# Performance work log

Measured on AMD Instinct MI355X. Metric: run time of the kernel, lower is better.

## Reference

```python
import jax, jax.numpy as jnp
import numpy as np

EMBED_DIM = 1024
NUM_HEADS = 16
HEAD_DIM = EMBED_DIM // NUM_HEADS
SCALE = HEAD_DIM ** -0.5


def setup_inputs() -> dict:
    key = jax.random.key(0)
    ks = jax.random.split(key, 9)
    B, S, D = 4, 2048, EMBED_DIM
    w_std = 1.0 / np.sqrt(D)
    x = jax.random.normal(ks[0], (B, S, D), dtype=jnp.float32)
    Wq = jax.random.uniform(ks[1], (D, D), jnp.float32, -w_std, w_std)
    bq = jax.random.uniform(ks[2], (D,), jnp.float32, -w_std, w_std)
    Wk = jax.random.uniform(ks[3], (D, D), jnp.float32, -w_std, w_std)
    bk = jax.random.uniform(ks[4], (D,), jnp.float32, -w_std, w_std)
    Wv = jax.random.uniform(ks[5], (D, D), jnp.float32, -w_std, w_std)
    bv = jax.random.uniform(ks[6], (D,), jnp.float32, -w_std, w_std)
    Wo = jax.random.uniform(ks[7], (D, D), jnp.float32, -w_std, w_std)
    bo = jax.random.uniform(ks[8], (D,), jnp.float32, -w_std, w_std)
    return {"x": x, "Wq": Wq, "bq": bq, "Wk": Wk, "bk": bk,
            "Wv": Wv, "bv": bv, "Wo": Wo, "bo": bo}


def reference(x, Wq, bq, Wk, bk, Wv, bv, Wo, bo):
    B, S, D = x.shape
    H, Dh = NUM_HEADS, HEAD_DIM
    # projections; Linear stores weight as [out,in] -> y = x @ W.T + b,
    # here W is stored as [D, D] used as x @ W + b (equivalent param'zation)
    q = (x @ Wq + bq).reshape(B, S, H, Dh).transpose(0, 2, 1, 3)  # [B,H,S,Dh]
    k = (x @ Wk + bk).reshape(B, S, H, Dh).transpose(0, 2, 1, 3)
    v = (x @ Wv + bv).reshape(B, S, H, Dh).transpose(0, 2, 1, 3)
    scores = jnp.einsum("bhqd,bhkd->bhqk", q, k) * SCALE  # [B,H,S,S]
    attn = jax.nn.softmax(scores, axis=-1)  # dropout is identity in eval mode
    out = jnp.einsum("bhqk,bhkd->bhqd", attn, v)  # [B,H,S,Dh]
    out = out.transpose(0, 2, 1, 3).reshape(B, S, D)
    return out @ Wo + bo
```

## Files before the change

### kernel.cpp

```cpp
#include <hip/hip_runtime.h>
#include <stdint.h>
#include <stddef.h>


typedef __attribute__((ext_vector_type(8)))  short          s16x8;
typedef __attribute__((ext_vector_type(8)))  unsigned short u16x8;
typedef __attribute__((ext_vector_type(4)))  unsigned short u16x4;
typedef __attribute__((ext_vector_type(4)))  float          f32x4;
typedef __attribute__((ext_vector_type(16))) float          f32x16;

#define DMODEL 1024
#define SEQ    2048
#define NHEAD  16
#define DHEAD  64
#define NTOK   8192
#define QSCALE 0.1803368801111244f

#define MFMA_B16(a, b, c) __builtin_amdgcn_mfma_f32_16x16x32_bf16((a), (b), (c), 0, 0, 0)
#define MFMA32(a, b, c)   __builtin_amdgcn_mfma_f32_32x32x16_bf16((a), (b), (c), 0, 0, 0)

__device__ __forceinline__ float bf2f(unsigned short u) {
  union { unsigned int i; float f; } v; v.i = ((unsigned int)u) << 16; return v.f;
}
__device__ __forceinline__ unsigned short f2bf(float f) {
  union { float f; unsigned int i; } v; v.f = f;
  unsigned int r = v.i + 0x7FFFu + ((v.i >> 16) & 1u);
  return (unsigned short)(r >> 16);
}
__device__ __forceinline__ float fexp2(float x) {
#if __has_builtin(__builtin_amdgcn_exp2f)
  return __builtin_amdgcn_exp2f(x);
#else
  return exp2f(x);
#endif
}
__device__ __forceinline__ unsigned int cvtpk(float a, float b) {
  unsigned int r;
  asm("v_cvt_pk_bf16_f32 %0, %1, %2" : "=v"(r) : "v"(a), "v"(b));
  return r;
}

__device__ __forceinline__ void gld16(const unsigned short* g, unsigned short* l) {
  __builtin_amdgcn_global_load_lds(
      (const __attribute__((address_space(1))) void*)g,
      (__attribute__((address_space(3))) void*)l, 16, 0, 0);
}

__global__ void detect_fp32(const unsigned short* __restrict__ w, int* __restrict__ flag) {
  __shared__ int cnt;
  if (threadIdx.x == 0) cnt = 0;
  __syncthreads();
  int local = 0;
  for (int i = threadIdx.x; i < 8192; i += 256) {
    const unsigned short v = w[i];
    if ((v & 0x7F80u) >= 0x3F80u) local++;
  }
  atomicAdd(&cnt, local);
  __syncthreads();
  if (threadIdx.x == 0) *flag = (cnt >= 128) ? 1 : 0;
}

__global__ void norm_vec4(const void* __restrict__ s0, const void* __restrict__ s1,
                          const void* __restrict__ s2, const void* __restrict__ s3,
                          unsigned short* __restrict__ d0, unsigned short* __restrict__ d1,
                          unsigned short* __restrict__ d2, unsigned short* __restrict__ d3,
                          const int* __restrict__ flag) {
  const int fl = *flag;
  const int v = blockIdx.y;
  const void* src = (v == 0) ? s0 : (v == 1) ? s1 : (v == 2) ? s2 : s3;
  unsigned short* dst = (v == 0) ? d0 : (v == 1) ? d1 : (v == 2) ? d2 : d3;
  const int i = blockIdx.x * 256 + threadIdx.x;
  dst[i] = fl ? f2bf(((const float*)src)[i]) : ((const unsigned short*)src)[i];
}

__global__ __launch_bounds__(256) void norm_x(const void* __restrict__ src,
                                              unsigned short* __restrict__ dst,
                                              const int* __restrict__ flag) {
  const int fl = *flag;
  const size_t i = ((size_t)blockIdx.x * 256 + threadIdx.x) * 8;
  if (fl) {
    const float* s = (const float*)src + i;
    u16x8 o;
#pragma unroll
    for (int j = 0; j < 8; ++j) o[j] = f2bf(s[j]);
    *(u16x8*)(dst + i) = o;
  } else {
    *(u16x8*)(dst + i) = *(const u16x8*)((const unsigned short*)src + i);
  }
}

__global__ __launch_bounds__(256) void transpose4(const void* __restrict__ i0,
                                                  const void* __restrict__ i1,
                                                  const void* __restrict__ i2,
                                                  const void* __restrict__ i3,
                                                  unsigned short* __restrict__ o0,
                                                  unsigned short* __restrict__ o1,
                                                  unsigned short* __restrict__ o2,
                                                  unsigned short* __restrict__ o3,
                                                  const int* __restrict__ flag) {
  __shared__ unsigned short tile[64][65];
  const int z = blockIdx.z;
  const void* in = (z == 0) ? i0 : (z == 1) ? i1 : (z == 2) ? i2 : i3;
  unsigned short* out = (z == 0) ? o0 : (z == 1) ? o1 : (z == 2) ? o2 : o3;
  const int fl = *flag;
  const int tx = threadIdx.x;
  const int ty = threadIdx.y;
  const int bx = blockIdx.x * 64;
  const int by = blockIdx.y * 64;
  const float* inf = (const float*)in;
  const unsigned short* inu = (const unsigned short*)in;
#pragma unroll
  for (int i = 0; i < 16; ++i) {
    const int r = i * 4 + ty;
    const size_t idx = (size_t)(by + r) * DMODEL + bx + tx;
    tile[r][tx] = fl ? f2bf(inf[idx]) : inu[idx];
  }
  __syncthreads();
#pragma unroll
  for (int i = 0; i < 16; ++i) {
    const int r = i * 4 + ty;
    out[(size_t)(bx + r) * DMODEL + by + tx] = tile[tx][r];
  }
}

template <int MODE>
__global__ __launch_bounds__(256) void gemm_bt(const unsigned short* __restrict__ A,
                                               const unsigned short* __restrict__ Bt,
                                               const unsigned short* __restrict__ bias0,
                                               const unsigned short* __restrict__ bias1,
                                               unsigned short* __restrict__ C0,
                                               unsigned short* __restrict__ C1,
                                               float* __restrict__ Cf) {
  __shared__ __align__(16) unsigned short As[128 * 32];
  __shared__ __align__(16) unsigned short Bs[128 * 32];

  const int t = threadIdx.x;
  const int wv = t >> 6;
  const int lane = t & 63;
  const int q4 = lane >> 4;
  const int c  = lane & 15;
  const int wm = wv >> 1;
  const int wn = wv & 1;
  const int m0 = blockIdx.x * 128;
  const int n0 = blockIdx.y * 128;

  f32x4 acc[4][4];
#pragma unroll
  for (int i = 0; i < 4; ++i)
#pragma unroll
    for (int j = 0; j < 4; ++j) acc[i][j] = (f32x4){0.f, 0.f, 0.f, 0.f};

  const int ch0 = wv * 128 + lane;
  const int ch1 = ch0 + 64;
  const unsigned short* Ag0 = A  + (size_t)(m0 + (ch0 >> 2)) * DMODEL + (ch0 & 3) * 8;
  const unsigned short* Ag1 = A  + (size_t)(m0 + (ch1 >> 2)) * DMODEL + (ch1 & 3) * 8;
  const unsigned short* Bg0 = Bt + (size_t)(n0 + (ch0 >> 2)) * DMODEL + (ch0 & 3) * 8;
  const unsigned short* Bg1 = Bt + (size_t)(n0 + (ch1 >> 2)) * DMODEL + (ch1 & 3) * 8;
  unsigned short* Al0 = As + (wv * 2 + 0) * 512;
  unsigned short* Al1 = As + (wv * 2 + 1) * 512;
  unsigned short* Bl0 = Bs + (wv * 2 + 0) * 512;
  unsigned short* Bl1 = Bs + (wv * 2 + 1) * 512;

  for (int k0 = 0; k0 < DMODEL; k0 += 32) {
    gld16(Ag0 + k0, Al0);
    gld16(Ag1 + k0, Al1);
    gld16(Bg0 + k0, Bl0);
    gld16(Bg1 + k0, Bl1);
    __syncthreads();

    s16x8 af[4], bfr[4];
#pragma unroll
    for (int i = 0; i < 4; ++i)
      af[i] = *(const s16x8*)(As + (wm * 64 + i * 16 + c) * 32 + q4 * 8);
#pragma unroll
    for (int j = 0; j < 4; ++j)
      bfr[j] = *(const s16x8*)(Bs + (wn * 64 + j * 16 + c) * 32 + q4 * 8);
    __builtin_amdgcn_s_setprio(1);
#pragma unroll
    for (int i = 0; i < 4; ++i)
#pragma unroll
      for (int j = 0; j < 4; ++j) acc[i][j] = MFMA_B16(af[i], bfr[j], acc[i][j]);
    __builtin_amdgcn_s_setprio(0);
    __syncthreads();
  }

  if (MODE == 2) {
#pragma unroll
    for (int i = 0; i < 4; ++i) {
#pragma unroll
      for (int rg = 0; rg < 4; ++rg) {
        const int m = m0 + wm * 64 + i * 16 + q4 * 4 + rg;
        const float bval = bf2f(bias0[m]);
#pragma unroll
        for (int j = 0; j < 4; ++j) {
          const int n = n0 + wn * 64 + j * 16 + c;
          C0[(((size_t)(n >> 11) * 1024 + m) << 11) + (n & 2047)] =
              f2bf(acc[i][j][rg] + bval);
        }
      }
    }
  } else {
#pragma unroll
    for (int j = 0; j < 4; ++j) {
      const int n = n0 + wn * 64 + j * 16 + c;
      float bval;
      if (MODE == 0) {
        bval = bf2f(bias0[n]);
      } else {
        bval = bf2f((n < 1024) ? bias0[n] : bias1[n & 1023]);
      }
#pragma unroll
      for (int i = 0; i < 4; ++i) {
#pragma unroll
        for (int rg = 0; rg < 4; ++rg) {
          const int m = m0 + wm * 64 + i * 16 + q4 * 4 + rg;
          const float oval = acc[i][j][rg] + bval;
          if (MODE == 0) {
            Cf[(size_t)m * DMODEL + n] = oval;
          } else {
            const int d = n & 1023;
            const int h = d >> 6, dh = d & 63;
            const int b = m >> 11, s = m & 2047;
            const size_t idx = ((((size_t)b * NHEAD + h) * SEQ + s) << 6) + dh;
            if (n < 1024) C0[idx] = f2bf(oval * QSCALE);
            else          C1[idx] = f2bf(oval);
          }
        }
      }
    }
  }
}

__global__ void copyout(const float* __restrict__ X, void* __restrict__ out,
                        const int* __restrict__ flag) {
  const int fl = *flag;
  const size_t i = (size_t)blockIdx.x * 1024 + threadIdx.x * 4;
#pragma unroll
  for (int j = 0; j < 4; ++j) {
    const float v = X[i + j];
    if (fl) ((float*)out)[i + j] = v;
    else    ((unsigned short*)out)[i + j] = f2bf(v);
  }
}

__global__ __launch_bounds__(256, 2) void attn_fused(const unsigned short* __restrict__ Qg,
                                                     const unsigned short* __restrict__ Kg,
                                                     const unsigned short* __restrict__ VTg,
                                                     unsigned short* __restrict__ Of) {
  __shared__ __align__(16) unsigned short smem[16384];

  const int t = threadIdx.x;
  const int wv = t >> 6;
  const int lane = t & 63;
  const int hi = lane >> 5;
  const int ql = lane & 31;
  const int bh = blockIdx.x;
  const int q0 = blockIdx.y * 256;
  const int b = bh >> 4, h = bh & 15;

  const unsigned short* Qb  = Qg  + ((size_t)bh * SEQ + q0 + wv * 64) * DHEAD;
  const unsigned short* Kb  = Kg  + (size_t)bh * SEQ * DHEAD;
  const unsigned short* VTb = VTg + (size_t)bh * DHEAD * SEQ;

  int koff[2], voff[2];
#pragma unroll
  for (int cl = 0; cl < 2; ++cl) {
    const int p = wv * 128 + cl * 64 + lane;
    const int row = p >> 3;
    const int slot = (p & 7) ^ (row & 7);
    koff[cl] = row * 64 + slot * 8;
    voff[cl] = row * 2048 + slot * 8;
  }
  int off[4];
#pragma unroll
  for (int s = 0; s < 4; ++s) off[s] = (((s * 2 + hi) ^ (ql & 7)) * 8);

  {
    unsigned short* Kd = smem;
    unsigned short* Vd = smem + 4096;
#pragma unroll
    for (int cl = 0; cl < 2; ++cl) {
      gld16(Kb + koff[cl], Kd + (wv * 128 + cl * 64) * 8);
      gld16(VTb + voff[cl], Vd + (wv * 128 + cl * 64) * 8);
    }
  }

  s16x8 qf[2][4];
#pragma unroll
  for (int qt = 0; qt < 2; ++qt)
#pragma unroll
    for (int s = 0; s < 4; ++s)
      qf[qt][s] = *(const s16x8*)(Qb + (size_t)(qt * 32 + ql) * DHEAD + s * 16 + hi * 8);

  f32x16 acco[2][2];
#pragma unroll
  for (int qt = 0; qt < 2; ++qt)
#pragma unroll
    for (int dt = 0; dt < 2; ++dt)
#pragma unroll
      for (int r = 0; r < 16; ++r) acco[qt][dt][r] = 0.f;
  f32x16 zv;
#pragma unroll
  for (int r = 0; r < 16; ++r) zv[r] = 0.f;
  float rs[2][4] = {{0.f, 0.f, 0.f, 0.f}, {0.f, 0.f, 0.f, 0.f}};

  for (int kt = 0; kt < SEQ / 64; ++kt) {
    __syncthreads();
    const int cur = kt & 1;
    if (kt + 1 < SEQ / 64) {
      unsigned short* Kd = smem + (cur ^ 1) * 8192;
      unsigned short* Vd = smem + (cur ^ 1) * 8192 + 4096;
      const unsigned short* Ksrc = Kb + (size_t)(kt + 1) * 64 * DHEAD;
      const unsigned short* Vsrc = VTb + (size_t)(kt + 1) * 64;
#pragma unroll
      for (int cl = 0; cl < 2; ++cl) {
        gld16(Ksrc + koff[cl], Kd + (wv * 128 + cl * 64) * 8);
        gld16(Vsrc + voff[cl], Vd + (wv * 128 + cl * 64) * 8);
      }
    }
    const unsigned short* Ksb = smem + cur * 8192;
    const unsigned short* Vtb = smem + cur * 8192 + 4096;

    f32x16 accs[2][2];
    __builtin_amdgcn_s_setprio(1);
#pragma unroll
    for (int k2 = 0; k2 < 2; ++k2) {
#pragma unroll
      for (int s = 0; s < 4; ++s) {
        const s16x8 kf = *(const s16x8*)(Ksb + (k2 * 32 + ql) * 64 + off[s]);
        if (s == 0) {
          accs[0][k2] = MFMA32(kf, qf[0][s], zv);
          accs[1][k2] = MFMA32(kf, qf[1][s], zv);
        } else {
          accs[0][k2] = MFMA32(kf, qf[0][s], accs[0][k2]);
          accs[1][k2] = MFMA32(kf, qf[1][s], accs[1][k2]);
        }
      }
    }
    __builtin_amdgcn_s_setprio(0);

    unsigned int u[2][2][8];
#pragma unroll
    for (int qt = 0; qt < 2; ++qt) {
#pragma unroll
      for (int k2 = 0; k2 < 2; ++k2) {
#pragma unroll
        for (int r = 0; r < 16; ++r) {
          const float p = fexp2(accs[qt][k2][r]);
          accs[qt][k2][r] = p;
          rs[qt][r & 3] += p;
        }
#pragma unroll
        for (int i = 0; i < 8; ++i)
          u[qt][k2][i] = cvtpk(accs[qt][k2][2 * i], accs[qt][k2][2 * i + 1]);
      }
    }

    __builtin_amdgcn_s_setprio(1);
#pragma unroll
    for (int k2 = 0; k2 < 2; ++k2) {
#pragma unroll
      for (int s = 0; s < 2; ++s) {
        const int kap = k2 * 2 + s;
        const s16x8 vf0 = *(const s16x8*)(Vtb + (0 * 32 + ql) * 64 + off[kap]);
        const s16x8 vf1 = *(const s16x8*)(Vtb + (1 * 32 + ql) * 64 + off[kap]);
#pragma unroll
        for (int qt = 0; qt < 2; ++qt) {
          unsigned int a0 = u[qt][k2][4 * s + 0], b0 = u[qt][k2][4 * s + 2];
          unsigned int a1 = u[qt][k2][4 * s + 1], b1 = u[qt][k2][4 * s + 3];
          asm("v_permlane32_swap_b32 %0, %1" : "+v"(a0), "+v"(b0));
          asm("v_permlane32_swap_b32 %0, %1" : "+v"(a1), "+v"(b1));
          union { unsigned int w[4]; s16x8 v; } pb;
          pb.w[0] = a0; pb.w[1] = a1; pb.w[2] = b0; pb.w[3] = b1;
          acco[qt][0] = MFMA32(vf0, pb.v, acco[qt][0]);
          acco[qt][1] = MFMA32(vf1, pb.v, acco[qt][1]);
        }
      }
    }
    __builtin_amdgcn_s_setprio(0);
  }

#pragma unroll
  for (int qt = 0; qt < 2; ++qt) {
    float lsum = (rs[qt][0] + rs[qt][1]) + (rs[qt][2] + rs[qt][3]);
    lsum += __shfl_xor(lsum, 32);
    const float inv = 1.0f / lsum;
    const int tok = q0 + wv * 64 + qt * 32 + ql;
    unsigned short* orow = Of + ((size_t)b * SEQ + tok) * DMODEL + h * DHEAD;
#pragma unroll
    for (int dt = 0; dt < 2; ++dt) {
#pragma unroll
      for (int rq = 0; rq < 4; ++rq) {
        u16x4 o;
#pragma unroll
        for (int j = 0; j < 4; ++j) o[j] = f2bf(acco[qt][dt][rq * 4 + j] * inv);
        *(u16x4*)(orow + dt * 32 + rq * 8 + hi * 4) = o;
      }
    }
  }
}

extern "C" void kernel_launch(void* const* d_in, const int* in_sizes, int n_in,
                              void* d_out, int out_size, void* d_ws, size_t ws_size,
                              hipStream_t stream) {
  const void* x  = d_in[0];
  const void* Wq = d_in[1];
  const void* bq = d_in[2];
  const void* Wk = d_in[3];
  const void* bk = d_in[4];
  const void* Wv = d_in[5];
  const void* bv = d_in[6];
  const void* Wo = d_in[7];
  const void* bo = d_in[8];

  unsigned short* ws = (unsigned short*)d_ws;
  const size_t M1 = (size_t)DMODEL * DMODEL;
  const size_t MQ = (size_t)NTOK * DMODEL;

  unsigned short* Qw  = ws;
  unsigned short* Kw  = Qw + MQ;
  unsigned short* Vw  = Kw + MQ;
  unsigned short* WqT = Vw + MQ;
  unsigned short* WkT = WqT + M1;
  unsigned short* WvT = WkT + M1;
  unsigned short* WoT = WvT + M1;
  unsigned short* bqn = WoT + M1;
  unsigned short* bkn = bqn + 1024;
  unsigned short* bvn = bkn + 1024;
  unsigned short* bon = bvn + 1024;
  int*            flg = (int*)(bon + 1024);
  float*          X   = (float*)Kw;
  unsigned short* Xb  = (unsigned short*)d_out;
  unsigned short* Ob  = (unsigned short*)d_out;

  detect_fp32<<<1, 256, 0, stream>>>((const unsigned short*)Wq, flg);

  norm_vec4<<<dim3(4, 4), 256, 0, stream>>>(bq, bk, bv, bo,
                                            bqn, bkn, bvn, bon, flg);

  transpose4<<<dim3(16, 16, 4), dim3(64, 4), 0, stream>>>(
      Wq, Wk, Wv, Wo, WqT, WkT, WvT, WoT, flg);

  norm_x<<<4096, 256, 0, stream>>>(x, Xb, flg);

  gemm_bt<1><<<dim3(64, 16), 256, 0, stream>>>(Xb, WqT, bqn, bkn, Qw, Kw, nullptr);
  gemm_bt<2><<<dim3(8, 64), 256, 0, stream>>>(WvT, Xb, bvn, nullptr, Vw, nullptr, nullptr);

  attn_fused<<<dim3(64, 8), 256, 0, stream>>>(Qw, Kw, Vw, Ob);

  gemm_bt<0><<<dim3(64, 8), 256, 0, stream>>>(Ob, WoT, bon, nullptr,
                                              nullptr, nullptr, X);
  copyout<<<8192, 256, 0, stream>>>(X, d_out, flg);
}
```

Before: 324.9 us.

## Double-buffer GEMM LDS tiles and add explicit vmcnt drains before barriers

The projection GEMM kernel now uses two LDS buffers for its A and B tiles. It prefetches the next K-slice with global_load_lds while the current slice is fed to MFMA, and one of the two barriers per iteration is removed. Explicit s_waitcnt vmcnt(0) drains are inserted before the barriers in both the GEMM and attention loops, so asynchronous LDS loads are complete before other waves read the data. LDS use per block doubles, which could lower occupancy, and the drain at the top of each iteration limits how much the load and compute actually overlap.

```diff
diff --git a/kernel.cpp b/kernel.cpp
--- a/kernel.cpp
+++ b/kernel.cpp
@@ -44,6 +44,9 @@
   __builtin_amdgcn_global_load_lds(
       (const __attribute__((address_space(1))) void*)g,
       (__attribute__((address_space(3))) void*)l, 16, 0, 0);
+}
+__device__ __forceinline__ void vmdrain() {
+  asm volatile("s_waitcnt vmcnt(0)" ::: "memory");
 }
 
 __global__ void detect_fp32(const unsigned short* __restrict__ w, int* __restrict__ flag) {
@@ -131,8 +134,8 @@
                                                unsigned short* __restrict__ C0,
                                                unsigned short* __restrict__ C1,
                                                float* __restrict__ Cf) {
-  __shared__ __align__(16) unsigned short As[128 * 32];
-  __shared__ __align__(16) unsigned short Bs[128 * 32];
+  __shared__ __align__(16) unsigned short As[2 * 128 * 32];
+  __shared__ __align__(16) unsigned short Bs[2 * 128 * 32];
 
   const int t = threadIdx.x;
   const int wv = t >> 6;
@@ -156,32 +159,42 @@
   const unsigned short* Ag1 = A  + (size_t)(m0 + (ch1 >> 2)) * DMODEL + (ch1 & 3) * 8;
   const unsigned short* Bg0 = Bt + (size_t)(n0 + (ch0 >> 2)) * DMODEL + (ch0 & 3) * 8;
   const unsigned short* Bg1 = Bt + (size_t)(n0 + (ch1 >> 2)) * DMODEL + (ch1 & 3) * 8;
-  unsigned short* Al0 = As + (wv * 2 + 0) * 512;
-  unsigned short* Al1 = As + (wv * 2 + 1) * 512;
-  unsigned short* Bl0 = Bs + (wv * 2 + 0) * 512;
-  unsigned short* Bl1 = Bs + (wv * 2 + 1) * 512;
+  const int lb0 = (wv * 2 + 0) * 512;
+  const int lb1 = (wv * 2 + 1) * 512;
+
+  gld16(Ag0, As + lb0);
+  gld16(Ag1, As + lb1);
+  gld16(Bg0, Bs + lb0);
+  gld16(Bg1, Bs + lb1);
 
   for (int k0 = 0; k0 < DMODEL; k0 += 32) {
-    gld16(Ag0 + k0, Al0);
-    gld16(Ag1 + k0, Al1);
-    gld16(Bg0 + k0, Bl0);
-    gld16(Bg1 + k0, Bl1);
+    const int cur = (k0 >> 5) & 1;
+    vmdrain();
     __syncthreads();
+    if (k0 + 32 < DMODEL) {
+      unsigned short* Ab = As + (cur ^ 1) * 4096;
+      unsigned short* Bb = Bs + (cur ^ 1) * 4096;
+      gld16(Ag0 + k0 + 32, Ab + lb0);
+      gld16(Ag1 + k0 + 32, Ab + lb1);
+      gld16(Bg0 + k0 + 32, Bb + lb0);
+      gld16(Bg1 + k0 + 32, Bb + lb1);
+    }
+    const unsigned short* Ac = As + cur * 4096;
+    const unsigned short* Bc = Bs + cur * 4096;
 
     s16x8 af[4], bfr[4];
 #pragma unroll
     for (int i = 0; i < 4; ++i)
-      af[i] = *(const s16x8*)(As + (wm * 64 + i * 16 + c) * 32 + q4 * 8);
+      af[i] = *(const s16x8*)(Ac + (wm * 64 + i * 16 + c) * 32 + q4 * 8);
 #pragma unroll
     for (int j = 0; j < 4; ++j)
-      bfr[j] = *(const s16x8*)(Bs + (wn * 64 + j * 16 + c) * 32 + q4 * 8);
+      bfr[j] = *(const s16x8*)(Bc + (wn * 64 + j * 16 + c) * 32 + q4 * 8);
     __builtin_amdgcn_s_setprio(1);
 #pragma unroll
     for (int i = 0; i < 4; ++i)
 #pragma unroll
       for (int j = 0; j < 4; ++j) acc[i][j] = MFMA_B16(af[i], bfr[j], acc[i][j]);
     __builtin_amdgcn_s_setprio(0);
-    __syncthreads();
   }
 
   if (MODE == 2) {
@@ -305,6 +318,7 @@
   float rs[2][4] = {{0.f, 0.f, 0.f, 0.f}, {0.f, 0.f, 0.f, 0.f}};
 
   for (int kt = 0; kt < SEQ / 64; ++kt) {
+    vmdrain();
     __syncthreads();
     const int cur = kt & 1;
     if (kt + 1 < SEQ / 64) {
```

New measurement: 305.0 us. -6.1%, faster.
